# Kernel optimization log

Hardware: AMD Instinct MI355X
Metric: run time of the kernel (lower is better)

Reference implementation:

```python
import jax, jax.numpy as jnp
import numpy as np


def setup_inputs() -> dict:
    key = jax.random.key(0)
    ks = jax.random.split(key, 5)
    B, C, H, W = 16, 512, 32, 32
    n_heads, d_k = 4, 128
    return {
        "x": jax.random.normal(ks[0], (B, C, H, W), dtype=jnp.float32),
        "w_proj": jax.random.normal(ks[1], (3 * n_heads * d_k, C), dtype=jnp.float32) * (1.0 / np.sqrt(C)),
        "b_proj": jax.random.normal(ks[2], (3 * n_heads * d_k,), dtype=jnp.float32) * 0.01,
        "w_out": jax.random.normal(ks[3], (C, n_heads * d_k), dtype=jnp.float32) * (1.0 / np.sqrt(n_heads * d_k)),
        "b_out": jax.random.normal(ks[4], (C,), dtype=jnp.float32) * 0.01,
        "n_heads": n_heads,
    }


def reference(x, w_proj, b_proj, w_out, b_out, n_heads):
    B, C, H, W = x.shape
    seq = H * W
    d_k = (w_proj.shape[0] // 3) // n_heads
    scale = d_k ** -0.5

    xs = x.reshape(B, C, seq).transpose(0, 2, 1)          # [B, seq, C]
    qkv = xs @ w_proj.T + b_proj                           # [B, seq, 3*H*d_k]
    qkv = qkv.reshape(B, seq, n_heads, 3 * d_k)
    q, k, v = jnp.split(qkv, 3, axis=-1)                   # each [B, seq, H, d_k]

    attn = jnp.einsum('bihd,bjhd->bijh', q, k) * scale     # [B, seq, seq, H]
    # NOTE: softmax over the QUERY axis (dim=1), faithful to the source quirk.
    attn = jax.nn.softmax(attn, axis=1)

    res = jnp.einsum('bijh,bjhd->bihd', attn, v)           # [B, seq, H, d_k]
    res = res.reshape(B, seq, n_heads * d_k)
    res = res @ w_out.T + b_out + xs                       # residual add
    return res.transpose(0, 2, 1).reshape(B, C, H, W)
```

## Files before the change

### kernel.cpp

```cpp
#include <hip/hip_runtime.h>
#include <hip/hip_bf16.h>
#include <math.h>

#define B_    16
#define CIN   512
#define SEQ   1024
#define NH    4
#define DK    128
#define OUT3  1536
#define SCALE 0.08838834764831845f

typedef __attribute__((ext_vector_type(8))) __bf16 bf16x8;
typedef __attribute__((ext_vector_type(4))) float f32x4;

#define MFMA(a, b, c) __builtin_amdgcn_mfma_f32_16x16x32_bf16((a), (b), (c), 0, 0, 0)

__device__ __forceinline__ ushort f2bf(float f) {
    __hip_bfloat16 h = __float2bfloat16(f);
    return *(ushort*)&h;
}
__device__ __forceinline__ uint pk2(float a, float b) {
    return (uint)f2bf(a) | ((uint)f2bf(b) << 16);
}
__device__ __forceinline__ void g2l16(const ushort* g, ushort* l) {
    __builtin_amdgcn_global_load_lds(
        (const __attribute__((address_space(1))) unsigned int*)g,
        (__attribute__((address_space(3))) unsigned int*)l, 16, 0, 0);
}
__device__ __forceinline__ int xcdswz(int bid, int nwg) {
    return (bid & 7) * (nwg >> 3) + (bid >> 3);
}

__global__ __launch_bounds__(256) void transpose_cast_kernel(
    const float* __restrict__ x, ushort* __restrict__ xt)
{
    __shared__ ushort t[64 * 66];
    const int tid = threadIdx.x;
    const int i0 = blockIdx.x * 64, c0 = blockIdx.y * 64, b = blockIdx.z;

    #pragma unroll
    for (int l = 0; l < 4; ++l) {
        int idx = tid + l * 256;
        int c = idx >> 4, i4 = (idx & 15) << 2;
        float4 v = *(const float4*)&x[((size_t)b * CIN + c0 + c) * SEQ + i0 + i4];
        t[(i4 + 0) * 66 + c] = f2bf(v.x);
        t[(i4 + 1) * 66 + c] = f2bf(v.y);
        t[(i4 + 2) * 66 + c] = f2bf(v.z);
        t[(i4 + 3) * 66 + c] = f2bf(v.w);
    }
    __syncthreads();
    #pragma unroll
    for (int l = 0; l < 4; ++l) {
        int idx = tid + l * 256;
        int i = idx >> 4, c4 = (idx & 15) << 2;
        uint2 p;
        p.x = *(const uint*)&t[i * 66 + c4];
        p.y = *(const uint*)&t[i * 66 + c4 + 2];
        *(uint2*)&xt[((size_t)b * SEQ + i0 + i) * CIN + c0 + c4] = p;
    }
}

__global__ __launch_bounds__(256) void cast_kernel(
    const float* __restrict__ src, ushort* __restrict__ dst, int n4)
{
    int idx = blockIdx.x * 256 + threadIdx.x;
    if (idx < n4) {
        float4 v = *(const float4*)&src[(size_t)idx * 4];
        uint2 p; p.x = pk2(v.x, v.y); p.y = pk2(v.z, v.w);
        *(uint2*)&dst[(size_t)idx * 4] = p;
    }
}

__global__ __launch_bounds__(256) void qkv_kernel(
    const ushort* __restrict__ wbf, const float* __restrict__ bias,
    const ushort* __restrict__ xt,
    ushort* __restrict__ qb, ushort* __restrict__ kb, ushort* __restrict__ vtb)
{
    __shared__ __attribute__((aligned(16))) ushort lds_a0[128 * 32];
    __shared__ __attribute__((aligned(16))) ushort lds_a1[128 * 32];
    __shared__ __attribute__((aligned(16))) ushort lds_b0[128 * 32];
    __shared__ __attribute__((aligned(16))) ushort lds_b1[128 * 32];
    const int tid = threadIdx.x;
    const int lane = tid & 63, wv = tid >> 6;
    const int l15 = lane & 15, l4 = lane >> 4;
    const int wm = wv >> 1, wn = wv & 1;
    const int swz = xcdswz(blockIdx.x, 1536);
    const int o0 = (swz % 12) * 128;
    const int i0 = ((swz / 12) & 7) * 128;
    const int b  = swz / 96;

    auto stage = [&](int c0, ushort* la, ushort* lb) {
        #pragma unroll
        for (int l = 0; l < 2; ++l) {
            int chunk = l * 256 + tid;
            int row = chunk >> 2, c = chunk & 3;
            g2l16(&wbf[(size_t)(o0 + row) * CIN + c0 + (c << 3)],
                  &la[(size_t)(l * 256 + wv * 64) * 8]);
        }
        #pragma unroll
        for (int l = 0; l < 2; ++l) {
            int chunk = l * 256 + tid;
            int row = chunk >> 2, c = chunk & 3;
            g2l16(&xt[((size_t)b * SEQ + i0 + row) * CIN + c0 + (c << 3)],
                  &lb[(size_t)(l * 256 + wv * 64) * 8]);
        }
    };

    f32x4 acc[4][4] = {};
    stage(0, lds_a0, lds_b0);
    __syncthreads();
    for (int it = 0; it < CIN / 32; ++it) {
        const ushort* la = (it & 1) ? lds_a1 : lds_a0;
        const ushort* lb = (it & 1) ? lds_b1 : lds_b0;
        if (it + 1 < CIN / 32)
            stage((it + 1) * 32, (it & 1) ? lds_a0 : lds_a1,
                                 (it & 1) ? lds_b0 : lds_b1);
        bf16x8 af[4], bfv[4];
        #pragma unroll
        for (int m = 0; m < 4; ++m)
            af[m] = *(const bf16x8*)&la[(wm * 64 + m * 16 + l15) * 32 + (l4 << 3)];
        #pragma unroll
        for (int n = 0; n < 4; ++n)
            bfv[n] = *(const bf16x8*)&lb[(wn * 64 + n * 16 + l15) * 32 + (l4 << 3)];
        #pragma unroll
        for (int m = 0; m < 4; ++m)
            #pragma unroll
            for (int n = 0; n < 4; ++n)
                acc[m][n] = MFMA(af[m], bfv[n], acc[m][n]);
        __syncthreads();
    }
    const int h = o0 / 384, which = (o0 % 384) / 128;
    const int bh = b * NH + h;
    #pragma unroll
    for (int m = 0; m < 4; ++m) {
        const int d0 = wm * 64 + m * 16 + (l4 << 2);
        float bia[4];
        #pragma unroll
        for (int r = 0; r < 4; ++r) bia[r] = bias[o0 + d0 + r];
        #pragma unroll
        for (int n = 0; n < 4; ++n) {
            const int i = i0 + wn * 64 + n * 16 + l15;
            float v0 = acc[m][n][0] + bia[0], v1 = acc[m][n][1] + bia[1];
            float v2 = acc[m][n][2] + bia[2], v3 = acc[m][n][3] + bia[3];
            if (which == 2) {
                vtb[((size_t)bh * DK + d0 + 0) * SEQ + i] = f2bf(v0);
                vtb[((size_t)bh * DK + d0 + 1) * SEQ + i] = f2bf(v1);
                vtb[((size_t)bh * DK + d0 + 2) * SEQ + i] = f2bf(v2);
                vtb[((size_t)bh * DK + d0 + 3) * SEQ + i] = f2bf(v3);
            } else {
                ushort* dst = (which == 0) ? qb : kb;
                uint2 p; p.x = pk2(v0, v1); p.y = pk2(v2, v3);
                *(uint2*)&dst[((size_t)bh * SEQ + i) * DK + d0] = p;
            }
        }
    }
}

__global__ __launch_bounds__(256) void stats_kernel(
    const ushort* __restrict__ qb, const ushort* __restrict__ kb,
    float* __restrict__ cstat)
{
    __shared__ __attribute__((aligned(16))) ushort lds_q0[64 * 128];
    __shared__ __attribute__((aligned(16))) ushort lds_q1[64 * 128];
    const int tid = threadIdx.x;
    const int lane = tid & 63, wv = tid >> 6;
    const int l15 = lane & 15, l4 = lane >> 4;
    const int swz = xcdswz(blockIdx.x, 512);
    const int bh = swz >> 3;
    const int j0 = (swz & 7) * 128 + wv * 32;
    const ushort* kbase = kb + (size_t)bh * SEQ * DK;
    const ushort* qbase = qb + (size_t)bh * SEQ * DK;

    auto stageQ = [&](int it, ushort* dst) {
        #pragma unroll
        for (int l = 0; l < 4; ++l) {
            int chunk = l * 256 + tid;
            int row = chunk >> 4, c = chunk & 15;
            g2l16(&qbase[(size_t)(it * 64 + row) * DK + ((c ^ (row & 7)) << 3)],
                  &dst[(size_t)(l * 256 + wv * 64) * 8]);
        }
    };

    bf16x8 kf[2][4];
    #pragma unroll
    for (int m = 0; m < 2; ++m)
        #pragma unroll
        for (int ks = 0; ks < 4; ++ks)
            kf[m][ks] = *(const bf16x8*)&kbase[(size_t)(j0 + m * 16 + l15) * DK
                                               + ks * 32 + (l4 << 3)];
    float mm[2][4], ss[2][4];
    #pragma unroll
    for (int m = 0; m < 2; ++m)
        #pragma unroll
        for (int r = 0; r < 4; ++r) { mm[m][r] = -1e30f; ss[m][r] = 0.0f; }

    stageQ(0, lds_q0);
    __syncthreads();
    for (int it = 0; it < SEQ / 64; ++it) {
        const ushort* lq = (it & 1) ? lds_q1 : lds_q0;
        if (it + 1 < SEQ / 64)
            stageQ(it + 1, (it & 1) ? lds_q0 : lds_q1);
        f32x4 sa0[4], sa1[4];
        __builtin_amdgcn_s_setprio(1);
        #pragma unroll
        for (int n = 0; n < 4; ++n) {
            f32x4 a0 = {}, a1 = {};
            #pragma unroll
            for (int ks = 0; ks < 4; ++ks) {
                bf16x8 bq = *(const bf16x8*)&lq[(n * 16 + l15) * 128
                                + ((((ks << 2) | l4) ^ (l15 & 7)) << 3)];
                a0 = MFMA(kf[0][ks], bq, a0);
                a1 = MFMA(kf[1][ks], bq, a1);
            }
            sa0[n] = a0; sa1[n] = a1;
        }
        __builtin_amdgcn_s_setprio(0);
        #pragma unroll
        for (int r = 0; r < 4; ++r) {
            {
                float v0 = sa0[0][r] * SCALE, v1 = sa0[1][r] * SCALE;
                float v2 = sa0[2][r] * SCALE, v3 = sa0[3][r] * SCALE;
                float tm = fmaxf(fmaxf(v0, v1), fmaxf(v2, v3));
                float nm = fmaxf(mm[0][r], tm);
                float s4 = __expf(v0 - nm) + __expf(v1 - nm)
                         + __expf(v2 - nm) + __expf(v3 - nm);
                ss[0][r] = ss[0][r] * __expf(mm[0][r] - nm) + s4;
                mm[0][r] = nm;
            }
            {
                float v0 = sa1[0][r] * SCALE, v1 = sa1[1][r] * SCALE;
                float v2 = sa1[2][r] * SCALE, v3 = sa1[3][r] * SCALE;
                float tm = fmaxf(fmaxf(v0, v1), fmaxf(v2, v3));
                float nm = fmaxf(mm[1][r], tm);
                float s4 = __expf(v0 - nm) + __expf(v1 - nm)
                         + __expf(v2 - nm) + __expf(v3 - nm);
                ss[1][r] = ss[1][r] * __expf(mm[1][r] - nm) + s4;
                mm[1][r] = nm;
            }
        }
        __syncthreads();
    }
    #pragma unroll
    for (int m = 0; m < 2; ++m)
        #pragma unroll
        for (int r = 0; r < 4; ++r) {
            float mv = mm[m][r], sv = ss[m][r];
            #pragma unroll
            for (int wmask = 1; wmask < 16; wmask <<= 1) {
                float mo = __shfl_xor(mv, wmask, 64);
                float so = __shfl_xor(sv, wmask, 64);
                float mn = fmaxf(mv, mo);
                sv = sv * __expf(mv - mn) + so * __expf(mo - mn);
                mv = mn;
            }
            if (l15 == 0) {
                int j = j0 + m * 16 + (l4 << 2) + r;
                cstat[(size_t)bh * SEQ + j] = mv + __logf(sv);
            }
        }
}

__global__ __launch_bounds__(256) void attn_kernel(
    const ushort* __restrict__ qb, const ushort* __restrict__ kb,
    const ushort* __restrict__ vtb, const float* __restrict__ cstat,
    ushort* __restrict__ resb)
{
    __shared__ __attribute__((aligned(16))) ushort lds_k[64 * 128];
    __shared__ __attribute__((aligned(16))) ushort lds_vt[128 * 64];
    __shared__ __attribute__((aligned(16))) ushort lds_p[64 * 72];
    const int tid = threadIdx.x;
    const int lane = tid & 63, wv = tid >> 6;
    const int l15 = lane & 15, l4 = lane >> 4;
    const int wj = wv & 1, wi = wv >> 1;
    const int swz = xcdswz(blockIdx.x, 1024);
    const int bh = swz >> 4, b = bh >> 2, h = bh & 3;
    const int i0 = (swz & 15) * 64;
    const ushort* qbase = qb + (size_t)bh * SEQ * DK;
    const ushort* kbase = kb + (size_t)bh * SEQ * DK;
    const ushort* vtbase = vtb + (size_t)bh * DK * SEQ;
    const float* cbase = cstat + (size_t)bh * SEQ;

    auto stageK = [&](int j0t) {
        #pragma unroll
        for (int l = 0; l < 4; ++l) {
            int chunk = l * 256 + tid;
            int row = chunk >> 4, c = chunk & 15;
            g2l16(&kbase[(size_t)(j0t + row) * DK + ((c ^ (row & 7)) << 3)],
                  &lds_k[(size_t)(l * 256 + wv * 64) * 8]);
        }
    };
    auto stageVt = [&](int j0t) {
        #pragma unroll
        for (int l = 0; l < 4; ++l) {
            int chunk = l * 256 + tid;
            int row = chunk >> 3, c = chunk & 7;
            g2l16(&vtbase[(size_t)row * SEQ + j0t + ((c ^ (row & 7)) << 3)],
                  &lds_vt[(size_t)(l * 256 + wv * 64) * 8]);
        }
    };

    bf16x8 qf[2][4];
    #pragma unroll
    for (int n = 0; n < 2; ++n)
        #pragma unroll
        for (int ks = 0; ks < 4; ++ks)
            qf[n][ks] = *(const bf16x8*)&qbase[(size_t)(i0 + wi * 32 + n * 16 + l15) * DK
                                               + ks * 32 + (l4 << 3)];
    f32x4 oacc[2][4] = {};

    stageK(0);
    __syncthreads();
    for (int jt = 0; jt < SEQ / 64; ++jt) {
        const int j0 = jt * 64;
        stageVt(j0);
        float4 cs0 = *(const float4*)&cbase[j0 + wj * 32 + (l4 << 2)];
        float4 cs1 = *(const float4*)&cbase[j0 + wj * 32 + 16 + (l4 << 2)];
        float cj[2][4] = {{cs0.x, cs0.y, cs0.z, cs0.w},
                          {cs1.x, cs1.y, cs1.z, cs1.w}};
        bf16x8 af[2][4];
        #pragma unroll
        for (int m = 0; m < 2; ++m)
            #pragma unroll
            for (int ks = 0; ks < 4; ++ks)
                af[m][ks] = *(const bf16x8*)&lds_k[(wj * 32 + m * 16 + l15) * 128
                                + ((((ks << 2) | l4) ^ (l15 & 7)) << 3)];
        __builtin_amdgcn_s_setprio(1);
        #pragma unroll
        for (int m = 0; m < 2; ++m)
            #pragma unroll
            for (int n = 0; n < 2; ++n) {
                f32x4 s = {};
                #pragma unroll
                for (int ks = 0; ks < 4; ++ks)
                    s = MFMA(af[m][ks], qf[n][ks], s);
                const int i = wi * 32 + n * 16 + l15;
                float p0 = __expf(s[0] * SCALE - cj[m][0]);
                float p1 = __expf(s[1] * SCALE - cj[m][1]);
                float p2 = __expf(s[2] * SCALE - cj[m][2]);
                float p3 = __expf(s[3] * SCALE - cj[m][3]);
                uint2 pp; pp.x = pk2(p0, p1); pp.y = pk2(p2, p3);
                *(uint2*)&lds_p[i * 72 + wj * 32 + m * 16 + (l4 << 2)] = pp;
            }
        __builtin_amdgcn_s_setprio(0);
        __syncthreads();
        if (jt + 1 < SEQ / 64) stageK(j0 + 64);
        __builtin_amdgcn_s_setprio(1);
        #pragma unroll
        for (int ks = 0; ks < 2; ++ks) {
            bf16x8 va0 = *(const bf16x8*)&lds_vt[(wv * 32 + l15) * 64
                            + ((((ks << 2) | l4) ^ (l15 & 7)) << 3)];
            bf16x8 va1 = *(const bf16x8*)&lds_vt[(wv * 32 + 16 + l15) * 64
                            + ((((ks << 2) | l4) ^ (l15 & 7)) << 3)];
            #pragma unroll
            for (int n = 0; n < 4; ++n) {
                bf16x8 pb = *(const bf16x8*)&lds_p[(n * 16 + l15) * 72
                                + ks * 32 + (l4 << 3)];
                oacc[0][n] = MFMA(va0, pb, oacc[0][n]);
                oacc[1][n] = MFMA(va1, pb, oacc[1][n]);
            }
        }
        __builtin_amdgcn_s_setprio(0);
        __syncthreads();
    }
    #pragma unroll
    for (int m = 0; m < 2; ++m)
        #pragma unroll
        for (int n = 0; n < 4; ++n) {
            const int i = i0 + n * 16 + l15;
            const int d = wv * 32 + m * 16 + (l4 << 2);
            uint2 p;
            p.x = pk2(oacc[m][n][0], oacc[m][n][1]);
            p.y = pk2(oacc[m][n][2], oacc[m][n][3]);
            *(uint2*)&resb[((size_t)b * SEQ + i) * (NH * DK) + h * DK + d] = p;
        }
}

__global__ __launch_bounds__(256) void outproj_kernel(
    const ushort* __restrict__ resb, const ushort* __restrict__ woutbf,
    const float* __restrict__ bout, const float* __restrict__ x,
    float* __restrict__ out)
{
    __shared__ __attribute__((aligned(16))) ushort lds_a0[128 * 32];
    __shared__ __attribute__((aligned(16))) ushort lds_a1[128 * 32];
    __shared__ __attribute__((aligned(16))) ushort lds_b0[128 * 32];
    __shared__ __attribute__((aligned(16))) ushort lds_b1[128 * 32];
    const int tid = threadIdx.x;
    const int lane = tid & 63, wv = tid >> 6;
    const int l15 = lane & 15, l4 = lane >> 4;
    const int wm = wv >> 1, wn = wv & 1;
    const int swz = xcdswz(blockIdx.x, 512);
    const int i0 = (swz & 7) * 128;
    const int c0 = ((swz >> 3) & 3) * 128;
    const int b  = swz >> 5;

    auto stage = [&](int k0, ushort* la, ushort* lb) {
        #pragma unroll
        for (int l = 0; l < 2; ++l) {
            int chunk = l * 256 + tid;
            int row = chunk >> 2, c = chunk & 3;
            g2l16(&woutbf[(size_t)(c0 + row) * (NH * DK) + k0 + (c << 3)],
                  &la[(size_t)(l * 256 + wv * 64) * 8]);
        }
        #pragma unroll
        for (int l = 0; l < 2; ++l) {
            int chunk = l * 256 + tid;
            int row = chunk >> 2, c = chunk & 3;
            g2l16(&resb[((size_t)b * SEQ + i0 + row) * (NH * DK) + k0 + (c << 3)],
                  &lb[(size_t)(l * 256 + wv * 64) * 8]);
        }
    };

    f32x4 acc[4][4] = {};
    stage(0, lds_a0, lds_b0);
    __syncthreads();
    for (int it = 0; it < (NH * DK) / 32; ++it) {
        const ushort* la = (it & 1) ? lds_a1 : lds_a0;
        const ushort* lb = (it & 1) ? lds_b1 : lds_b0;
        if (it + 1 < (NH * DK) / 32)
            stage((it + 1) * 32, (it & 1) ? lds_a0 : lds_a1,
                                 (it & 1) ? lds_b0 : lds_b1);
        bf16x8 af[4], bfv[4];
        #pragma unroll
        for (int m = 0; m < 4; ++m)
            af[m] = *(const bf16x8*)&la[(wm * 64 + m * 16 + l15) * 32 + (l4 << 3)];
        #pragma unroll
        for (int n = 0; n < 4; ++n)
            bfv[n] = *(const bf16x8*)&lb[(wn * 64 + n * 16 + l15) * 32 + (l4 << 3)];
        #pragma unroll
        for (int m = 0; m < 4; ++m)
            #pragma unroll
            for (int n = 0; n < 4; ++n)
                acc[m][n] = MFMA(af[m], bfv[n], acc[m][n]);
        __syncthreads();
    }
    #pragma unroll
    for (int m = 0; m < 4; ++m) {
        const int cb = c0 + wm * 64 + m * 16 + (l4 << 2);
        float bia[4];
        #pragma unroll
        for (int r = 0; r < 4; ++r) bia[r] = bout[cb + r];
        #pragma unroll
        for (int n = 0; n < 4; ++n) {
            const int i = i0 + wn * 64 + n * 16 + l15;
            #pragma unroll
            for (int r = 0; r < 4; ++r) {
                size_t off = ((size_t)b * CIN + cb + r) * SEQ + i;
                out[off] = acc[m][n][r] + bia[r] + x[off];
            }
        }
    }
}

extern "C" void kernel_launch(void* const* d_in, const int* in_sizes, int n_in,
                              void* d_out, int out_size, void* d_ws, size_t ws_size,
                              hipStream_t stream) {
    const float* x      = (const float*)d_in[0];
    const float* w_proj = (const float*)d_in[1];
    const float* b_proj = (const float*)d_in[2];
    const float* w_out  = (const float*)d_in[3];
    const float* b_out  = (const float*)d_in[4];

    const size_t xtE = (size_t)B_ * SEQ * CIN;
    const size_t qkE = (size_t)B_ * NH * SEQ * DK;
    ushort* xt    = (ushort*)d_ws;
    ushort* qb    = xt + xtE;
    ushort* kb    = qb + qkE;
    ushort* vtb   = kb + qkE;
    float*  cstat = (float*)(vtb + qkE);
    ushort* resb  = (ushort*)(cstat + 2 * (size_t)B_ * NH * SEQ);
    ushort* wobf  = resb + (size_t)B_ * SEQ * (NH * DK);
    ushort* wpbf  = resb;
    float*  out   = (float*)d_out;

    transpose_cast_kernel<<<dim3(SEQ / 64, CIN / 64, B_), 256, 0, stream>>>(x, xt);
    cast_kernel<<<dim3(768), 256, 0, stream>>>(w_proj, wpbf, 196608);
    cast_kernel<<<dim3(256), 256, 0, stream>>>(w_out, wobf, 65536);
    qkv_kernel<<<dim3(1536), 256, 0, stream>>>(wpbf, b_proj, xt, qb, kb, vtb);
    stats_kernel<<<dim3(512), 256, 0, stream>>>(qb, kb, cstat);
    attn_kernel<<<dim3(1024), 256, 0, stream>>>(qb, kb, vtb, cstat, resb);
    outproj_kernel<<<dim3(512), 256, 0, stream>>>(resb, wobf, b_out, x, out);
}
```

Baseline: 250.2 us.

## Double-buffer V/P in attention and use fixed-shift softmax column stats

```diff
diff --git a/kernel.cpp b/kernel.cpp
--- a/kernel.cpp
+++ b/kernel.cpp
@@ -9,6 +9,7 @@
 #define DK    128
 #define OUT3  1536
 #define SCALE 0.08838834764831845f
+#define CSHIFT 8.0f
 
 typedef __attribute__((ext_vector_type(8))) __bf16 bf16x8;
 typedef __attribute__((ext_vector_type(4))) float f32x4;
@@ -188,11 +189,7 @@
         for (int ks = 0; ks < 4; ++ks)
             kf[m][ks] = *(const bf16x8*)&kbase[(size_t)(j0 + m * 16 + l15) * DK
                                                + ks * 32 + (l4 << 3)];
-    float mm[2][4], ss[2][4];
-    #pragma unroll
-    for (int m = 0; m < 2; ++m)
-        #pragma unroll
-        for (int r = 0; r < 4; ++r) { mm[m][r] = -1e30f; ss[m][r] = 0.0f; }
+    float ss[2][4] = {};
 
     stageQ(0, lds_q0);
     __syncthreads();
@@ -217,26 +214,14 @@
         __builtin_amdgcn_s_setprio(0);
         #pragma unroll
         for (int r = 0; r < 4; ++r) {
-            {
-                float v0 = sa0[0][r] * SCALE, v1 = sa0[1][r] * SCALE;
-                float v2 = sa0[2][r] * SCALE, v3 = sa0[3][r] * SCALE;
-                float tm = fmaxf(fmaxf(v0, v1), fmaxf(v2, v3));
-                float nm = fmaxf(mm[0][r], tm);
-                float s4 = __expf(v0 - nm) + __expf(v1 - nm)
-                         + __expf(v2 - nm) + __expf(v3 - nm);
-                ss[0][r] = ss[0][r] * __expf(mm[0][r] - nm) + s4;
-                mm[0][r] = nm;
-            }
-            {
-                float v0 = sa1[0][r] * SCALE, v1 = sa1[1][r] * SCALE;
-                float v2 = sa1[2][r] * SCALE, v3 = sa1[3][r] * SCALE;
-                float tm = fmaxf(fmaxf(v0, v1), fmaxf(v2, v3));
-                float nm = fmaxf(mm[1][r], tm);
-                float s4 = __expf(v0 - nm) + __expf(v1 - nm)
-                         + __expf(v2 - nm) + __expf(v3 - nm);
-                ss[1][r] = ss[1][r] * __expf(mm[1][r] - nm) + s4;
-                mm[1][r] = nm;
-            }
+            float e0 = 0.0f, e1 = 0.0f;
+            #pragma unroll
+            for (int n = 0; n < 4; ++n) {
+                e0 += __expf(fmaf(sa0[n][r], SCALE, -CSHIFT));
+                e1 += __expf(fmaf(sa1[n][r], SCALE, -CSHIFT));
+            }
+            ss[0][r] += e0;
+            ss[1][r] += e1;
         }
         __syncthreads();
     }
@@ -244,18 +229,13 @@
     for (int m = 0; m < 2; ++m)
         #pragma unroll
         for (int r = 0; r < 4; ++r) {
-            float mv = mm[m][r], sv = ss[m][r];
-            #pragma unroll
-            for (int wmask = 1; wmask < 16; wmask <<= 1) {
-                float mo = __shfl_xor(mv, wmask, 64);
-                float so = __shfl_xor(sv, wmask, 64);
-                float mn = fmaxf(mv, mo);
-                sv = sv * __expf(mv - mn) + so * __expf(mo - mn);
-                mv = mn;
-            }
+            float sv = ss[m][r];
+            #pragma unroll
+            for (int wmask = 1; wmask < 16; wmask <<= 1)
+                sv += __shfl_xor(sv, wmask, 64);
             if (l15 == 0) {
                 int j = j0 + m * 16 + (l4 << 2) + r;
-                cstat[(size_t)bh * SEQ + j] = mv + __logf(sv);
+                cstat[(size_t)bh * SEQ + j] = CSHIFT + __logf(sv);
             }
         }
 }
@@ -265,9 +245,10 @@
     const ushort* __restrict__ vtb, const float* __restrict__ cstat,
     ushort* __restrict__ resb)
 {
-    __shared__ __attribute__((aligned(16))) ushort lds_k[64 * 128];
-    __shared__ __attribute__((aligned(16))) ushort lds_vt[128 * 64];
-    __shared__ __attribute__((aligned(16))) ushort lds_p[64 * 72];
+    __shared__ __attribute__((aligned(16))) ushort lds_vt0[128 * 64];
+    __shared__ __attribute__((aligned(16))) ushort lds_vt1[128 * 64];
+    __shared__ __attribute__((aligned(16))) ushort lds_p0[64 * 72];
+    __shared__ __attribute__((aligned(16))) ushort lds_p1[64 * 72];
     const int tid = threadIdx.x;
     const int lane = tid & 63, wv = tid >> 6;
     const int l15 = lane & 15, l4 = lane >> 4;
@@ -280,22 +261,23 @@
     const ushort* vtbase = vtb + (size_t)bh * DK * SEQ;
     const float* cbase = cstat + (size_t)bh * SEQ;
 
-    auto stageK = [&](int j0t) {
-        #pragma unroll
-        for (int l = 0; l < 4; ++l) {
-            int chunk = l * 256 + tid;
-            int row = chunk >> 4, c = chunk & 15;
-            g2l16(&kbase[(size_t)(j0t + row) * DK + ((c ^ (row & 7)) << 3)],
-                  &lds_k[(size_t)(l * 256 + wv * 64) * 8]);
-        }
-    };
-    auto stageVt = [&](int j0t) {
+    auto loadK = [&](bf16x8 (&kf)[2][4], int jt) {
+        const ushort* kr = kbase + (size_t)(jt * 64 + wj * 32) * DK;
+        #pragma unroll
+        for (int m = 0; m < 2; ++m)
+            #pragma unroll
+            for (int ks = 0; ks < 4; ++ks)
+                kf[m][ks] = *(const bf16x8*)&kr[(size_t)(m * 16 + l15) * DK
+                                                + ks * 32 + (l4 << 3)];
+    };
+    auto stageVt = [&](ushort* dst, int jt) {
+        const int j0t = jt * 64;
         #pragma unroll
         for (int l = 0; l < 4; ++l) {
             int chunk = l * 256 + tid;
             int row = chunk >> 3, c = chunk & 7;
             g2l16(&vtbase[(size_t)row * SEQ + j0t + ((c ^ (row & 7)) << 3)],
-                  &lds_vt[(size_t)(l * 256 + wv * 64) * 8]);
+                  &dst[(size_t)(l * 256 + wv * 64) * 8]);
         }
     };
 
@@ -308,22 +290,12 @@
                                                + ks * 32 + (l4 << 3)];
     f32x4 oacc[2][4] = {};
 
-    stageK(0);
-    __syncthreads();
-    for (int jt = 0; jt < SEQ / 64; ++jt) {
-        const int j0 = jt * 64;
-        stageVt(j0);
-        float4 cs0 = *(const float4*)&cbase[j0 + wj * 32 + (l4 << 2)];
-        float4 cs1 = *(const float4*)&cbase[j0 + wj * 32 + 16 + (l4 << 2)];
-        float cj[2][4] = {{cs0.x, cs0.y, cs0.z, cs0.w},
-                          {cs1.x, cs1.y, cs1.z, cs1.w}};
-        bf16x8 af[2][4];
-        #pragma unroll
-        for (int m = 0; m < 2; ++m)
-            #pragma unroll
-            for (int ks = 0; ks < 4; ++ks)
-                af[m][ks] = *(const bf16x8*)&lds_k[(wj * 32 + m * 16 + l15) * 128
-                                + ((((ks << 2) | l4) ^ (l15 & 7)) << 3)];
+    auto phaseA = [&](bf16x8 (&kf)[2][4], int jt, ushort* pbuf) {
+        const float* cb = cbase + jt * 64 + wj * 32;
+        float4 cs0 = *(const float4*)&cb[(l4 << 2)];
+        float4 cs1 = *(const float4*)&cb[16 + (l4 << 2)];
+        float nc[2][4] = {{-cs0.x, -cs0.y, -cs0.z, -cs0.w},
+                          {-cs1.x, -cs1.y, -cs1.z, -cs1.w}};
         __builtin_amdgcn_s_setprio(1);
         #pragma unroll
         for (int m = 0; m < 2; ++m)
@@ -332,35 +304,50 @@
                 f32x4 s = {};
                 #pragma unroll
                 for (int ks = 0; ks < 4; ++ks)
-                    s = MFMA(af[m][ks], qf[n][ks], s);
+                    s = MFMA(kf[m][ks], qf[n][ks], s);
                 const int i = wi * 32 + n * 16 + l15;
-                float p0 = __expf(s[0] * SCALE - cj[m][0]);
-                float p1 = __expf(s[1] * SCALE - cj[m][1]);
-                float p2 = __expf(s[2] * SCALE - cj[m][2]);
-                float p3 = __expf(s[3] * SCALE - cj[m][3]);
+                float p0 = __expf(fmaf(s[0], SCALE, nc[m][0]));
+                float p1 = __expf(fmaf(s[1], SCALE, nc[m][1]));
+                float p2 = __expf(fmaf(s[2], SCALE, nc[m][2]));
+                float p3 = __expf(fmaf(s[3], SCALE, nc[m][3]));
                 uint2 pp; pp.x = pk2(p0, p1); pp.y = pk2(p2, p3);
-                *(uint2*)&lds_p[i * 72 + wj * 32 + m * 16 + (l4 << 2)] = pp;
+                *(uint2*)&pbuf[i * 72 + wj * 32 + m * 16 + (l4 << 2)] = pp;
             }
         __builtin_amdgcn_s_setprio(0);
-        __syncthreads();
-        if (jt + 1 < SEQ / 64) stageK(j0 + 64);
+    };
+    auto phaseB = [&](const ushort* vt, const ushort* pbuf) {
         __builtin_amdgcn_s_setprio(1);
         #pragma unroll
         for (int ks = 0; ks < 2; ++ks) {
-            bf16x8 va0 = *(const bf16x8*)&lds_vt[(wv * 32 + l15) * 64
+            bf16x8 va0 = *(const bf16x8*)&vt[(wv * 32 + l15) * 64
                             + ((((ks << 2) | l4) ^ (l15 & 7)) << 3)];
-            bf16x8 va1 = *(const bf16x8*)&lds_vt[(wv * 32 + 16 + l15) * 64
+            bf16x8 va1 = *(const bf16x8*)&vt[(wv * 32 + 16 + l15) * 64
                             + ((((ks << 2) | l4) ^ (l15 & 7)) << 3)];
             #pragma unroll
             for (int n = 0; n < 4; ++n) {
-                bf16x8 pb = *(const bf16x8*)&lds_p[(n * 16 + l15) * 72
+                bf16x8 pb = *(const bf16x8*)&pbuf[(n * 16 + l15) * 72
                                 + ks * 32 + (l4 << 3)];
                 oacc[0][n] = MFMA(va0, pb, oacc[0][n]);
                 oacc[1][n] = MFMA(va1, pb, oacc[1][n]);
             }
         }
         __builtin_amdgcn_s_setprio(0);
+    };
+
+    bf16x8 kfA[2][4], kfB[2][4];
+    loadK(kfA, 0);
+    stageVt(lds_vt0, 0);
+    for (int t = 0; t < SEQ / 64; t += 2) {
+        loadK(kfB, t + 1);
+        phaseA(kfA, t, lds_p0);
         __syncthreads();
+        stageVt(lds_vt1, t + 1);
+        phaseB(lds_vt0, lds_p0);
+        if (t + 2 < SEQ / 64) loadK(kfA, t + 2);
+        phaseA(kfB, t + 1, lds_p1);
+        __syncthreads();
+        if (t + 2 < SEQ / 64) stageVt(lds_vt0, t + 2);
+        phaseB(lds_vt1, lds_p1);
     }
     #pragma unroll
     for (int m = 0; m < 2; ++m)
```

New measurement: 283.2 us. +13.2%, slower.

## Use fixed-shift softmax statistics and XOR-swizzled P tile in LDS

Applied to the files above, without the earlier changes.

```diff
diff --git a/kernel.cpp b/kernel.cpp
--- a/kernel.cpp
+++ b/kernel.cpp
@@ -9,6 +9,7 @@
 #define DK    128
 #define OUT3  1536
 #define SCALE 0.08838834764831845f
+#define CSHIFT 8.0f
 
 typedef __attribute__((ext_vector_type(8))) __bf16 bf16x8;
 typedef __attribute__((ext_vector_type(4))) float f32x4;
@@ -188,11 +189,7 @@
         for (int ks = 0; ks < 4; ++ks)
             kf[m][ks] = *(const bf16x8*)&kbase[(size_t)(j0 + m * 16 + l15) * DK
                                                + ks * 32 + (l4 << 3)];
-    float mm[2][4], ss[2][4];
-    #pragma unroll
-    for (int m = 0; m < 2; ++m)
-        #pragma unroll
-        for (int r = 0; r < 4; ++r) { mm[m][r] = -1e30f; ss[m][r] = 0.0f; }
+    float ss[2][4] = {};
 
     stageQ(0, lds_q0);
     __syncthreads();
@@ -217,26 +214,14 @@
         __builtin_amdgcn_s_setprio(0);
         #pragma unroll
         for (int r = 0; r < 4; ++r) {
-            {
-                float v0 = sa0[0][r] * SCALE, v1 = sa0[1][r] * SCALE;
-                float v2 = sa0[2][r] * SCALE, v3 = sa0[3][r] * SCALE;
-                float tm = fmaxf(fmaxf(v0, v1), fmaxf(v2, v3));
-                float nm = fmaxf(mm[0][r], tm);
-                float s4 = __expf(v0 - nm) + __expf(v1 - nm)
-                         + __expf(v2 - nm) + __expf(v3 - nm);
-                ss[0][r] = ss[0][r] * __expf(mm[0][r] - nm) + s4;
-                mm[0][r] = nm;
-            }
-            {
-                float v0 = sa1[0][r] * SCALE, v1 = sa1[1][r] * SCALE;
-                float v2 = sa1[2][r] * SCALE, v3 = sa1[3][r] * SCALE;
-                float tm = fmaxf(fmaxf(v0, v1), fmaxf(v2, v3));
-                float nm = fmaxf(mm[1][r], tm);
-                float s4 = __expf(v0 - nm) + __expf(v1 - nm)
-                         + __expf(v2 - nm) + __expf(v3 - nm);
-                ss[1][r] = ss[1][r] * __expf(mm[1][r] - nm) + s4;
-                mm[1][r] = nm;
-            }
+            float e0 = 0.0f, e1 = 0.0f;
+            #pragma unroll
+            for (int n = 0; n < 4; ++n) {
+                e0 += __expf(fmaf(sa0[n][r], SCALE, -CSHIFT));
+                e1 += __expf(fmaf(sa1[n][r], SCALE, -CSHIFT));
+            }
+            ss[0][r] += e0;
+            ss[1][r] += e1;
         }
         __syncthreads();
     }
@@ -244,18 +229,13 @@
     for (int m = 0; m < 2; ++m)
         #pragma unroll
         for (int r = 0; r < 4; ++r) {
-            float mv = mm[m][r], sv = ss[m][r];
-            #pragma unroll
-            for (int wmask = 1; wmask < 16; wmask <<= 1) {
-                float mo = __shfl_xor(mv, wmask, 64);
-                float so = __shfl_xor(sv, wmask, 64);
-                float mn = fmaxf(mv, mo);
-                sv = sv * __expf(mv - mn) + so * __expf(mo - mn);
-                mv = mn;
-            }
+            float sv = ss[m][r];
+            #pragma unroll
+            for (int wmask = 1; wmask < 16; wmask <<= 1)
+                sv += __shfl_xor(sv, wmask, 64);
             if (l15 == 0) {
                 int j = j0 + m * 16 + (l4 << 2) + r;
-                cstat[(size_t)bh * SEQ + j] = mv + __logf(sv);
+                cstat[(size_t)bh * SEQ + j] = CSHIFT + __logf(sv);
             }
         }
 }
@@ -267,7 +247,7 @@
 {
     __shared__ __attribute__((aligned(16))) ushort lds_k[64 * 128];
     __shared__ __attribute__((aligned(16))) ushort lds_vt[128 * 64];
-    __shared__ __attribute__((aligned(16))) ushort lds_p[64 * 72];
+    __shared__ __attribute__((aligned(16))) ushort lds_p[64 * 64];
     const int tid = threadIdx.x;
     const int lane = tid & 63, wv = tid >> 6;
     const int l15 = lane & 15, l4 = lane >> 4;
@@ -315,8 +295,8 @@
         stageVt(j0);
         float4 cs0 = *(const float4*)&cbase[j0 + wj * 32 + (l4 << 2)];
         float4 cs1 = *(const float4*)&cbase[j0 + wj * 32 + 16 + (l4 << 2)];
-        float cj[2][4] = {{cs0.x, cs0.y, cs0.z, cs0.w},
-                          {cs1.x, cs1.y, cs1.z, cs1.w}};
+        float nc[2][4] = {{-cs0.x, -cs0.y, -cs0.z, -cs0.w},
+                          {-cs1.x, -cs1.y, -cs1.z, -cs1.w}};
         bf16x8 af[2][4];
         #pragma unroll
         for (int m = 0; m < 2; ++m)
@@ -334,12 +314,14 @@
                 for (int ks = 0; ks < 4; ++ks)
                     s = MFMA(af[m][ks], qf[n][ks], s);
                 const int i = wi * 32 + n * 16 + l15;
-                float p0 = __expf(s[0] * SCALE - cj[m][0]);
-                float p1 = __expf(s[1] * SCALE - cj[m][1]);
-                float p2 = __expf(s[2] * SCALE - cj[m][2]);
-                float p3 = __expf(s[3] * SCALE - cj[m][3]);
+                float p0 = __expf(fmaf(s[0], SCALE, nc[m][0]));
+                float p1 = __expf(fmaf(s[1], SCALE, nc[m][1]));
+                float p2 = __expf(fmaf(s[2], SCALE, nc[m][2]));
+                float p3 = __expf(fmaf(s[3], SCALE, nc[m][3]));
                 uint2 pp; pp.x = pk2(p0, p1); pp.y = pk2(p2, p3);
-                *(uint2*)&lds_p[i * 72 + wj * 32 + m * 16 + (l4 << 2)] = pp;
+                const int c8 = wj * 4 + m * 2 + (l4 >> 1);
+                *(uint2*)((char*)lds_p + i * 128
+                          + ((c8 ^ (i & 7)) << 4) + ((l4 & 1) << 3)) = pp;
             }
         __builtin_amdgcn_s_setprio(0);
         __syncthreads();
@@ -353,8 +335,10 @@
                             + ((((ks << 2) | l4) ^ (l15 & 7)) << 3)];
             #pragma unroll
             for (int n = 0; n < 4; ++n) {
-                bf16x8 pb = *(const bf16x8*)&lds_p[(n * 16 + l15) * 72
-                                + ks * 32 + (l4 << 3)];
+                const int row = n * 16 + l15;
+                const int c8 = ks * 4 + l4;
+                bf16x8 pb = *(const bf16x8*)((const char*)lds_p + row * 128
+                                + ((c8 ^ (row & 7)) << 4));
                 oacc[0][n] = MFMA(va0, pb, oacc[0][n]);
                 oacc[1][n] = MFMA(va1, pb, oacc[1][n]);
             }
```

After: 239.2 us. -4.4%, faster.
